# Kernel tuning notes

Hardware: AMD Instinct MI355X
Metric: run time of the kernel (lower is better)

The kernel has to match this reference:

```python
import jax, jax.numpy as jnp
import numpy as np
from jax import lax

B, N, H, D = 4, 384, 8, 5          # graphs, nodes/graph, heads, max multi-hop dist
NE, E_TOT, DH, L = 2048, 8192, 256, 10  # edges/graph, total real edges, d_hidden, curve samples
N_SPATIAL, N_EDGE_DIST = 64, 128


def _bn(x, g, b):
    # eval-mode BatchNorm1d (running_mean=0, running_var=1): affine only
    return x * g + b


def _conv1d(x, w):
    # x: [E, C, L], w: [O, I, 3], SAME padding, stride 1
    return lax.conv_general_dilated(x, w, (1,), 'SAME',
                                    dimension_numbers=('NCH', 'OIH', 'NCH'))


def setup_inputs() -> dict:
    key = jax.random.key(0)
    ks = iter(jax.random.split(key, 64))
    nrm = lambda shape, s=0.02: jax.random.normal(next(ks), shape, jnp.float32) * s
    std = 0.02 / np.sqrt(12.0)  # init_params with n_layer=12 for Linear weights
    inp = {}
    inp['attn_bias'] = jax.random.normal(next(ks), (B, N + 1, N + 1), jnp.float32)
    inp['spatial_pos'] = jax.random.randint(next(ks), (B, N, N), 0, N_SPATIAL)
    inp['d2_dist'] = jax.random.normal(next(ks), (B, N, N, 32), jnp.float32)
    inp['a3_dist'] = jax.random.normal(next(ks), (B, N, N, 32), jnp.float32)
    inp['edge_data'] = jax.random.normal(next(ks), (E_TOT, L, 7), jnp.float32)
    inp['edge_path'] = jax.random.randint(next(ks), (B, N, N, D), 0, NE + 1)
    inp['edge_padding_mask'] = jnp.zeros((B, NE), bool)  # all real edges
    inp['src'] = jax.random.randint(next(ks), (E_TOT,), 0, B * N)
    inp['dst'] = jax.random.randint(next(ks), (E_TOT,), 0, B * N)
    inp['node_data'] = jax.random.normal(next(ks), (B * N, DH), jnp.float32)
    # --- parameters ---
    inp['spatial_emb'] = nrm((N_SPATIAL, H)).at[0].set(0.0)  # padding_idx=0
    inp['t_virtual'] = nrm((1, H))
    inp['w_d2'] = nrm((H, 32), std); inp['b_d2'] = jnp.zeros((H,), jnp.float32)
    inp['w_a3'] = nrm((H, 32), std); inp['b_a3'] = jnp.zeros((H,), jnp.float32)
    inp['cw1'] = nrm((64, 7, 3), std);  inp['cg1'] = jnp.ones((64,));  inp['cb1'] = jnp.zeros((64,))
    inp['cw2'] = nrm((128, 64, 3), std); inp['cg2'] = jnp.ones((128,)); inp['cb2'] = jnp.zeros((128,))
    inp['cw3'] = nrm((256, 128, 3), std); inp['cg3'] = jnp.ones((256,)); inp['cb3'] = jnp.zeros((256,))
    inp['cw_out'] = nrm((H, 256), std)
    # _EdgeConv (UV-Net style): proj Linear(d_hidden->H), MLP(H->64->H), BN, GIN eps
    inp['wp'] = nrm((H, DH), std); inp['bp'] = jnp.zeros((H,))
    inp['w1'] = nrm((64, H), std); inp['b1'] = jnp.zeros((64,))
    inp['g1'] = jnp.ones((64,)); inp['bb1'] = jnp.zeros((64,))
    inp['w2'] = nrm((H, 64), std); inp['b2'] = jnp.zeros((H,))
    inp['g_out'] = jnp.ones((H,)); inp['bb_out'] = jnp.zeros((H,))
    inp['eps'] = jnp.zeros((), jnp.float32)
    inp['edge_dis_w'] = nrm((N_EDGE_DIST * H * H, 1))
    return inp


def reference(attn_bias, spatial_pos, d2_dist, a3_dist, edge_data, edge_path,
              edge_padding_mask, src, dst, node_data, spatial_emb, t_virtual,
              w_d2, b_d2, w_a3, b_a3, cw1, cg1, cb1, cw2, cg2, cb2, cw3, cg3, cb3,
              cw_out, wp, bp, w1, b1, g1, bb1, w2, b2, g_out, bb_out, eps, edge_dis_w):
    gab = jnp.repeat(attn_bias[:, None], H, axis=1)            # [B,H,N+1,N+1]
    spb = spatial_emb[spatial_pos]                              # [B,N,N,H]
    d2b = d2_dist @ w_d2.T + b_d2                               # [B,N,N,H]
    a3b = a3_dist @ w_a3.T + b_a3                               # [B,N,N,H]
    # CurveEncoder on per-edge curve samples
    x = jnp.transpose(edge_data, (0, 2, 1))                     # [E,7,L]
    x = jax.nn.leaky_relu(_bn(_conv1d(x, cw1), cg1[:, None], cb1[:, None]))
    x = jax.nn.leaky_relu(_bn(_conv1d(x, cw2), cg2[:, None], cb2[:, None]))
    x = jax.nn.leaky_relu(_bn(_conv1d(x, cw3), cg3[:, None], cb3[:, None]))
    ef = jnp.mean(x, axis=-1) @ cw_out.T                        # [E,H]
    # _EdgeConv: combine endpoint node features with edge features
    proj = node_data @ wp.T + bp                                # [B*N,H]
    h = (1.0 + eps) * ef + proj[src] + proj[dst]
    h = jax.nn.relu(_bn(h @ w1.T + b1, g1, bb1)) @ w2.T + b2
    edge_out = jax.nn.relu(_bn(h, g_out, bb_out))               # [E,H]
    # scatter real-edge features into padded table (row NE stays zero = padding)
    valid = (~edge_padding_mask).reshape(-1)                    # [B*NE]
    gidx = jnp.maximum(jnp.cumsum(valid) - 1, 0)
    vals = jnp.where(valid[:, None], edge_out[gidx], 0.0).reshape(B, NE, H)
    edge_feature = jnp.zeros((B, NE + 1, H), edge_out.dtype).at[:, :NE].set(vals)
    # gather along multi-hop paths, per-distance head mixing (bmm), normalize
    ep = edge_path.reshape(B, N * N * D)
    edge_input = jax.vmap(lambda f, p: f[p])(edge_feature, ep)  # [B,N*N*D,H]
    edge_input = edge_input.reshape(B, N, N, D, H)
    wdis = edge_dis_w.reshape(-1, H, H)[:D]                     # [D,H,H]
    edge_input = jnp.einsum('bijdh,dhk->bijdk', edge_input, wdis)
    sp = jnp.where(spatial_pos == 0, 1, spatial_pos)
    sp = jnp.where(sp > 1, sp - 1, sp)
    sp = jnp.clip(sp, 0, D)
    edge_bias = edge_input.sum(-2) / sp[..., None].astype(edge_input.dtype)
    inner = spb + d2b + a3b + edge_bias                         # [B,N,N,H]
    gab = gab.at[:, :, 1:, 1:].add(jnp.transpose(inner, (0, 3, 1, 2)))
    t = t_virtual.reshape(1, H, 1)
    gab = gab.at[:, :, 1:, 0].add(t)
    gab = gab.at[:, :, 0, :].add(t)
    return gab + attn_bias[:, None]
```

## Files before the change

### kernel.cpp

```cpp
#include <hip/hip_runtime.h>

#define NB    4
#define NNODE 384
#define NH    8
#define ND    5
#define NEDGE 2048
#define NEP1  2049
#define ETOT  8192
#define DHID  256
#define NP1   385
#define SQ1   (NP1*NP1)
#define NPOS  98304
#define NPOS2 (NPOS + 2)

typedef __attribute__((ext_vector_type(8)))  short short8;
typedef __attribute__((ext_vector_type(16))) float float16;

__device__ __forceinline__ unsigned short f2bf(float f) {
    union { float f; unsigned int u; } v; v.f = f;
    unsigned int u = v.u;
    return (unsigned short)((u + 0x7FFFu + ((u >> 16) & 1u)) >> 16);
}
__device__ __forceinline__ unsigned pkbf(float a, float b) {
    return (unsigned)f2bf(a) | ((unsigned)f2bf(b) << 16);
}
__device__ __forceinline__ short8 mk8(unsigned a, unsigned b, unsigned c, unsigned d) {
    union { unsigned u[4]; short8 s; } x; x.u[0]=a; x.u[1]=b; x.u[2]=c; x.u[3]=d; return x.s;
}
__device__ __forceinline__ float leaky(float v) { return v > 0.f ? v : 0.01f * v; }
__device__ __forceinline__ float16 zero16() {
    float16 z;
#pragma unroll
    for (int i = 0; i < 16; ++i) z[i] = 0.f;
    return z;
}
__device__ __forceinline__ void gl_lds16(const void* g, void* l) {
    __builtin_amdgcn_global_load_lds(
        (const __attribute__((address_space(1))) unsigned int*)g,
        (__attribute__((address_space(3))) unsigned int*)l,
        16, 0, 0);
}

__global__ __launch_bounds__(256) void prep_kernel(
    const float* __restrict__ cw1, const float* __restrict__ cw2, const float* __restrict__ cw3,
    const float* __restrict__ cw_out,
    const float* __restrict__ node_data, const float* __restrict__ wp, const float* __restrict__ bp,
    unsigned short* __restrict__ W1f, unsigned short* __restrict__ W2f, unsigned short* __restrict__ W3f,
    unsigned short* __restrict__ Wof,
    float* __restrict__ proj, float* __restrict__ edge_feature)
{
    int gid = blockIdx.x * 256 + threadIdx.x;
    if (gid < 98304) {
        int j = gid & 7, lane = (gid >> 3) & 63, blk = gid >> 9;
        int ks = blk & 7, tp = (blk >> 3) % 3, mt = blk / 24;
        int oc = mt * 32 + (lane & 31);
        int ic = ks * 16 + (lane >> 5) * 8 + j;
        W3f[gid] = f2bf(cw3[(oc * 128 + ic) * 3 + tp]);
    } else if (gid < 122880) {
        int f = gid - 98304;
        int j = f & 7, lane = (f >> 3) & 63, blk = f >> 9;
        int ks = blk & 3, tp = (blk >> 2) % 3, mt = blk / 12;
        int oc = mt * 32 + (lane & 31);
        int ic = ks * 16 + (lane >> 5) * 8 + j;
        W2f[f] = f2bf(cw2[(oc * 64 + ic) * 3 + tp]);
    } else if (gid < 124928) {
        int f = gid - 122880;
        int j = f & 7, lane = (f >> 3) & 63, blk = f >> 9;
        int ks = blk & 1, mt = blk >> 1;
        int oc = mt * 32 + (lane & 31);
        int k = ks * 16 + (lane >> 5) * 8 + j;
        int tp = k >> 3, c = k & 7;
        float v = (tp < 3 && c < 7) ? cw1[oc * 21 + c * 3 + tp] : 0.f;
        W1f[f] = f2bf(v);
    } else if (gid < 137216) {
        int f = gid - 124928;
        int v = f >> 3, h = f & 7;
        const float* nd = node_data + (size_t)v * DHID;
        const float* ww = wp + h * DHID;
        float acc = bp[h];
#pragma unroll 4
        for (int c = 0; c < DHID; c += 4)
            acc += nd[c]*ww[c] + nd[c+1]*ww[c+1] + nd[c+2]*ww[c+2] + nd[c+3]*ww[c+3];
        proj[f] = acc;
    } else if (gid < 137248) {
        int f = gid - 137216;
        int b = f >> 3, h = f & 7;
        edge_feature[((size_t)b * NEP1 + NEDGE) * NH + h] = 0.f;
    } else if (gid < 145440) {
        int f = gid - 137248;
        int j = f & 7, lane = (f >> 3) & 63, g = f >> 9;
        int m = lane & 31;
        int k = g * 16 + (lane >> 5) * 8 + j;
        Wof[f] = (m < 8) ? f2bf(cw_out[m * 256 + k]) : (unsigned short)0;
    }
}

#define X0_GROWS 8
__global__ __launch_bounds__(256) void pack_kernel(
    const float* __restrict__ edge_data,
    unsigned short* __restrict__ X0buf, unsigned short* __restrict__ X1buf,
    unsigned short* __restrict__ X2buf)
{
    int gid = blockIdx.x * 256 + threadIdx.x;
    const int NX0 = (NPOS + 2 * X0_GROWS) * 8;
    if (gid < NX0) {
        int row = gid >> 3, ch = gid & 7;
        int pos = row - X0_GROWS;
        unsigned short v = 0;
        if (pos >= 0 && pos < NPOS && ch < 7) {
            int pm = pos % 12;
            if (pm >= 1 && pm <= 10)
                v = f2bf(edge_data[(size_t)(pos / 12) * 70 + (pm - 1) * 7 + ch]);
        }
        X0buf[gid] = v;
    } else if (gid < NX0 + 128) {
        int f = gid - NX0;
        int p = f >> 5, rest = f & 31;
        int row = (rest >> 4) ? (NPOS + 1) : 0, col = rest & 15;
        X1buf[((size_t)p * NPOS2 + row) * 16 + col] = 0;
    } else if (gid < NX0 + 128 + 256) {
        int f = gid - NX0 - 128;
        int p = f >> 5, rest = f & 31;
        int row = (rest >> 4) ? (NPOS + 1) : 0, col = rest & 15;
        X2buf[((size_t)p * NPOS2 + row) * 16 + col] = 0;
    }
}

__global__ __launch_bounds__(256, 4) void conv1_kernel(
    const unsigned short* __restrict__ X0, const unsigned short* __restrict__ W1f,
    const float* __restrict__ cg1, const float* __restrict__ cb1,
    unsigned short* __restrict__ X1)
{
    const int t = threadIdx.x, wv = t >> 6, lane = t & 63;
    const int q = lane >> 5, n = lane & 31;
    const int pos = blockIdx.x * 128 + wv * 32 + n;

    float16 acc0 = zero16(), acc1 = zero16();
#pragma unroll
    for (int ks = 0; ks < 2; ++ks) {
        short8 b  = *(const short8*)(X0 + (pos - 1 + 2 * ks + q) * 8);
        short8 a0 = *(const short8*)(W1f + ((0 * 2 + ks) * 64 + lane) * 8);
        short8 a1 = *(const short8*)(W1f + ((1 * 2 + ks) * 64 + lane) * 8);
        acc0 = __builtin_amdgcn_mfma_f32_32x32x16_bf16(a0, b, acc0, 0, 0, 0);
        acc1 = __builtin_amdgcn_mfma_f32_32x32x16_bf16(a1, b, acc1, 0, 0, 0);
    }
    int pm = pos % 12;
    bool valid = (pm != 0) && (pm != 11);
#pragma unroll
    for (int mt = 0; mt < 2; ++mt) {
        const float16& acc = mt ? acc1 : acc0;
#pragma unroll
        for (int r2 = 0; r2 < 4; ++r2) {
            int oc0 = mt * 32 + 8 * r2 + 4 * q;
            float4 g4 = *(const float4*)(cg1 + oc0);
            float4 b4 = *(const float4*)(cb1 + oc0);
            unsigned short uu[4];
            uu[0] = valid ? f2bf(leaky(acc[r2*4+0] * g4.x + b4.x)) : (unsigned short)0;
            uu[1] = valid ? f2bf(leaky(acc[r2*4+1] * g4.y + b4.y)) : (unsigned short)0;
            uu[2] = valid ? f2bf(leaky(acc[r2*4+2] * g4.z + b4.z)) : (unsigned short)0;
            uu[3] = valid ? f2bf(leaky(acc[r2*4+3] * g4.w + b4.w)) : (unsigned short)0;
            uint2 pk; pk.x = uu[0] | ((unsigned)uu[1] << 16); pk.y = uu[2] | ((unsigned)uu[3] << 16);
            *(uint2*)(void*)(X1 + ((size_t)(oc0 >> 4) * NPOS2 + pos + 1) * 16 + (oc0 & 15)) = pk;
        }
    }
}

__global__ __launch_bounds__(256, 3) void conv2_kernel(
    const unsigned short* __restrict__ X1, const unsigned short* __restrict__ W2f,
    const float* __restrict__ cg2, const float* __restrict__ cb2,
    unsigned short* __restrict__ X2)
{
    __shared__ __align__(16) unsigned short sB[2][1568];
    const int t = threadIdx.x, wv = t >> 6, lane = t & 63;
    const int q = lane >> 5, n = lane & 31;
    const int base = blockIdx.x * 96;
    const int cbase = (wv < 3) ? wv * 64 : 132;

    gl_lds16(X1 + ((size_t)0 * NPOS2 + base) * 16 + (cbase + lane) * 8,
             &sB[0][cbase * 8]);

    float16 acc[3];
#pragma unroll
    for (int nt = 0; nt < 3; ++nt) acc[nt] = zero16();

    __syncthreads();

#pragma unroll
    for (int ks = 0; ks < 4; ++ks) {
        if (ks < 3)
            gl_lds16(X1 + ((size_t)(ks + 1) * NPOS2 + base) * 16 + (cbase + lane) * 8,
                     &sB[(ks + 1) & 1][cbase * 8]);
        const unsigned short* bb = sB[ks & 1];
#pragma unroll
        for (int tp = 0; tp < 3; ++tp) {
            short8 a = *(const short8*)(W2f + (((wv * 3 + tp) * 4 + ks) * 64 + lane) * 8);
#pragma unroll
            for (int nt = 0; nt < 3; ++nt) {
                short8 b = *(const short8*)(bb + (nt * 32 + n + tp) * 16 + q * 8);
                acc[nt] = __builtin_amdgcn_mfma_f32_32x32x16_bf16(a, b, acc[nt], 0, 0, 0);
            }
        }
        __syncthreads();
    }

#pragma unroll
    for (int nt = 0; nt < 3; ++nt) {
        int pos = base + nt * 32 + n;
        int pm = pos % 12;
        bool valid = (pm != 0) && (pm != 11);
#pragma unroll
        for (int r2 = 0; r2 < 4; ++r2) {
            int oc0 = wv * 32 + 8 * r2 + 4 * q;
            float4 g4 = *(const float4*)(cg2 + oc0);
            float4 b4 = *(const float4*)(cb2 + oc0);
            unsigned short uu[4];
            uu[0] = valid ? f2bf(leaky(acc[nt][r2*4+0] * g4.x + b4.x)) : (unsigned short)0;
            uu[1] = valid ? f2bf(leaky(acc[nt][r2*4+1] * g4.y + b4.y)) : (unsigned short)0;
            uu[2] = valid ? f2bf(leaky(acc[nt][r2*4+2] * g4.z + b4.z)) : (unsigned short)0;
            uu[3] = valid ? f2bf(leaky(acc[nt][r2*4+3] * g4.w + b4.w)) : (unsigned short)0;
            uint2 pk; pk.x = uu[0] | ((unsigned)uu[1] << 16); pk.y = uu[2] | ((unsigned)uu[3] << 16);
            *(uint2*)(void*)(X2 + ((size_t)(oc0 >> 4) * NPOS2 + pos + 1) * 16 + (oc0 & 15)) = pk;
        }
    }
}

__global__ __launch_bounds__(256, 2) void conv3_kernel(
    const unsigned short* __restrict__ X2, const unsigned short* __restrict__ W3f,
    const unsigned short* __restrict__ Wof,
    const float* __restrict__ cg3, const float* __restrict__ cb3,
    const int* __restrict__ src, const int* __restrict__ dst,
    const float* __restrict__ w1, const float* __restrict__ b1,
    const float* __restrict__ g1, const float* __restrict__ bb1,
    const float* __restrict__ w2, const float* __restrict__ b2,
    const float* __restrict__ g_out, const float* __restrict__ bb_out,
    const float* __restrict__ eps, const float* __restrict__ proj,
    float* __restrict__ edge_feature)
{
    __shared__ float fs[3072 + 64 + 512];
    __shared__ __align__(16) unsigned short sB[2][1568];
    const int t = threadIdx.x, wv = t >> 6, lane = t & 63;
    const int q = lane >> 5, n = lane & 31;
    const int base = blockIdx.x * 96;
    const int cbase = (wv < 3) ? wv * 64 : 132;

    gl_lds16(X2 + ((size_t)0 * NPOS2 + base) * 16 + (cbase + lane) * 8,
             &sB[0][cbase * 8]);

    float16 acc[2][3];
#pragma unroll
    for (int i = 0; i < 2; ++i)
#pragma unroll
        for (int nt = 0; nt < 3; ++nt) acc[i][nt] = zero16();

    __syncthreads();

#pragma unroll
    for (int ks = 0; ks < 8; ++ks) {
        if (ks < 7)
            gl_lds16(X2 + ((size_t)(ks + 1) * NPOS2 + base) * 16 + (cbase + lane) * 8,
                     &sB[(ks + 1) & 1][cbase * 8]);
        const unsigned short* bb = sB[ks & 1];
#pragma unroll
        for (int tp = 0; tp < 3; ++tp) {
            short8 a0 = *(const short8*)(W3f + ((((wv*2+0) * 3 + tp) * 8 + ks) * 64 + lane) * 8);
            short8 a1 = *(const short8*)(W3f + ((((wv*2+1) * 3 + tp) * 8 + ks) * 64 + lane) * 8);
#pragma unroll
            for (int nt = 0; nt < 3; ++nt) {
                short8 b = *(const short8*)(bb + (nt * 32 + n + tp) * 16 + q * 8);
                acc[0][nt] = __builtin_amdgcn_mfma_f32_32x32x16_bf16(a0, b, acc[0][nt], 0, 0, 0);
                acc[1][nt] = __builtin_amdgcn_mfma_f32_32x32x16_bf16(a1, b, acc[1][nt], 0, 0, 0);
            }
        }
        __syncthreads();
    }

    short8 wof[4];
#pragma unroll
    for (int g = 0; g < 4; ++g)
        wof[g] = *(const short8*)(Wof + ((wv * 4 + g) * 64 + lane) * 8);

#pragma unroll
    for (int nt = 0; nt < 3; ++nt) {
        int pm = (nt * 32 + n) % 12;
        bool valid = (pm != 0) && (pm != 11);
        float16 p = zero16();
#pragma unroll
        for (int i = 0; i < 2; ++i) {
            int mt = wv * 2 + i;
            float av[16];
#pragma unroll
            for (int r2 = 0; r2 < 4; ++r2) {
                int oc0 = mt * 32 + 8 * r2 + 4 * q;
                float4 g4 = *(const float4*)(cg3 + oc0);
                float4 b4 = *(const float4*)(cb3 + oc0);
                av[r2*4+0] = valid ? leaky(acc[i][nt][r2*4+0] * g4.x + b4.x) : 0.f;
                av[r2*4+1] = valid ? leaky(acc[i][nt][r2*4+1] * g4.y + b4.y) : 0.f;
                av[r2*4+2] = valid ? leaky(acc[i][nt][r2*4+2] * g4.z + b4.z) : 0.f;
                av[r2*4+3] = valid ? leaky(acc[i][nt][r2*4+3] * g4.w + b4.w) : 0.f;
            }
            unsigned pk[8], op[8];
#pragma unroll
            for (int z = 0; z < 8; ++z) pk[z] = pkbf(av[2*z], av[2*z+1]);
#pragma unroll
            for (int z = 0; z < 8; ++z) op[z] = __shfl_xor((int)pk[z], 32);
            short8 f0 = q == 0 ? mk8(pk[0], pk[1], op[0], op[1])
                               : mk8(op[2], op[3], pk[2], pk[3]);
            short8 f1 = q == 0 ? mk8(pk[4], pk[5], op[4], op[5])
                               : mk8(op[6], op[7], pk[6], pk[7]);
            p = __builtin_amdgcn_mfma_f32_32x32x16_bf16(wof[i*2+0], f0, p, 0, 0, 0);
            p = __builtin_amdgcn_mfma_f32_32x32x16_bf16(wof[i*2+1], f1, p, 0, 0, 0);
        }
        float4 st = make_float4(p[0], p[1], p[2], p[3]);
        *(float4*)&fs[((wv * 96) + nt * 32 + n) * 8 + 4 * q] = st;
    }
    __syncthreads();

    if (t < 64) {
        int e = t >> 3, h = t & 7;
        float s = 0.f;
#pragma unroll
        for (int w = 0; w < 4; ++w)
#pragma unroll 4
            for (int l = 0; l < 12; ++l) s += fs[(w * 96 + e * 12 + l) * 8 + h];
        float efv = 0.1f * s;
        int ge = blockIdx.x * 8 + e;
        fs[3072 + e * 8 + h] = (1.f + eps[0]) * efv
                             + proj[src[ge] * NH + h] + proj[dst[ge] * NH + h];
    }
    __syncthreads();

#pragma unroll
    for (int bb = 0; bb < 512; bb += 256) {
        int idx = bb + t;
        int e = idx >> 6, o = idx & 63;
        float a = b1[o];
#pragma unroll
        for (int h = 0; h < 8; ++h) a += fs[3072 + e * 8 + h] * w1[o * 8 + h];
        float v = a * g1[o] + bb1[o];
        fs[3136 + e * 64 + o] = v > 0.f ? v : 0.f;
    }
    __syncthreads();

    if (t < 64) {
        int e = t >> 3, h = t & 7;
        float a = b2[h];
#pragma unroll 8
        for (int o = 0; o < 64; ++o) a += fs[3136 + e * 64 + o] * w2[h * 64 + o];
        float v = a * g_out[h] + bb_out[h];
        v = v > 0.f ? v : 0.f;
        int ge = blockIdx.x * 8 + e;
        int b = ge >> 11, el2 = ge & (NEDGE - 1);
        edge_feature[((size_t)b * NEP1 + el2) * NH + h] = v;
    }
}

__global__ __launch_bounds__(256) void tbl_kernel(
    const float* __restrict__ edge_feature, const float* __restrict__ edge_dis_w,
    float* __restrict__ T)
{
    int idx = blockIdx.x * 256 + threadIdx.x;
    if (idx >= NEP1 * 8) return;
    int pi = idx >> 3, k = idx & 7;
    int d = blockIdx.y, b = blockIdx.z;
    const float* ef = edge_feature + ((size_t)b * NEP1 + pi) * NH;
    const float* w  = edge_dis_w + d * 64 + k;
    float s = 0.f;
#pragma unroll
    for (int h = 0; h < 8; ++h) s += ef[h] * w[h * 8];
    T[(((size_t)b * ND + d) * NEP1 + pi) * 8 + k] = s;
}

__global__ __launch_bounds__(256) void bias_kernel(
    const float* __restrict__ attn_bias, const int* __restrict__ spatial_pos,
    const float* __restrict__ d2_dist, const float* __restrict__ a3_dist,
    const int* __restrict__ edge_path,
    const float* __restrict__ spatial_emb, const float* __restrict__ t_virtual,
    const float* __restrict__ w_d2, const float* __restrict__ b_d2,
    const float* __restrict__ w_a3, const float* __restrict__ b_a3,
    const float* __restrict__ Tbl,
    float* __restrict__ out)
{
    __shared__ __align__(16) float s_emb[512];
    __shared__ __align__(16) float s_wd2[256];
    __shared__ __align__(16) float s_wa3[256];
    __shared__ float s_t[8], s_bd2[8], s_ba3[8];

    int t = threadIdx.x;
    for (int i = t; i < 512; i += 256) s_emb[i] = spatial_emb[i];
    if (t < 256) { s_wd2[t] = w_d2[t]; s_wa3[t] = w_a3[t]; }
    if (t < 8) { s_t[t] = t_virtual[t]; s_bd2[t] = b_d2[t]; s_ba3[t] = b_a3[t]; }
    __syncthreads();

    int gc = blockIdx.x * 32 + (t >> 3);
    int part = t & 7;
    if (gc >= NB * SQ1) return;
    int b   = gc / SQ1;
    int rem = gc % SQ1;
    int i = rem / NP1, j = rem % NP1;

    float base = 2.f * attn_bias[gc];
    bool border = (i == 0) || (j == 0);
    int r = border ? 0 : i - 1, c = border ? 0 : j - 1;
    size_t nidx = ((size_t)b * NNODE + r) * NNODE + c;
    int sp = spatial_pos[nidx];

    float acc[8];
    {
        float4 vd = ((const float4*)(d2_dist + nidx * 32))[part];
        float4 va = ((const float4*)(a3_dist + nidx * 32))[part];
        const float4* wd2 = (const float4*)s_wd2;
        const float4* wa3 = (const float4*)s_wa3;
#pragma unroll
        for (int h = 0; h < 8; ++h) {
            float4 w4 = wd2[h * 8 + part];
            float4 v4 = wa3[h * 8 + part];
            acc[h] = vd.x*w4.x + vd.y*w4.y + vd.z*w4.z + vd.w*w4.w
                   + va.x*v4.x + va.y*v4.y + va.z*v4.z + va.w*v4.w;
        }
    }

    float edp = 0.f;
    const int* ep = edge_path + nidx * ND;
    const float* Tb = Tbl + (size_t)b * (ND * NEP1 * 8);
#pragma unroll
    for (int d = 0; d < ND; ++d) {
        int pi = ep[d];
        edp += Tb[((size_t)d * NEP1 + pi) * 8 + part];
    }
    int spd = (sp == 0) ? 1 : sp;
    spd = (spd > 1) ? spd - 1 : spd;
    spd = (spd > ND) ? ND : spd;
    float inv = 1.f / (float)spd;

#pragma unroll
    for (int m = 1; m < 8; m <<= 1) {
#pragma unroll
        for (int h = 0; h < 8; ++h) acc[h] += __shfl_xor(acc[h], m, 64);
    }

    float val = border ? (base + s_t[part])
                       : (base + acc[part] + edp * inv
                          + s_emb[sp * 8 + part] + s_bd2[part] + s_ba3[part]);
    out[((size_t)b * NH + part) * SQ1 + (size_t)i * NP1 + j] = val;
}

extern "C" void kernel_launch(void* const* d_in, const int* in_sizes, int n_in,
                              void* d_out, int out_size, void* d_ws, size_t ws_size,
                              hipStream_t stream)
{
    const float* attn_bias   = (const float*)d_in[0];
    const int*   spatial_pos = (const int*)  d_in[1];
    const float* d2_dist     = (const float*)d_in[2];
    const float* a3_dist     = (const float*)d_in[3];
    const float* edge_data   = (const float*)d_in[4];
    const int*   edge_path   = (const int*)  d_in[5];
    const int*   src         = (const int*)  d_in[7];
    const int*   dst         = (const int*)  d_in[8];
    const float* node_data   = (const float*)d_in[9];
    const float* spatial_emb = (const float*)d_in[10];
    const float* t_virtual   = (const float*)d_in[11];
    const float* w_d2        = (const float*)d_in[12];
    const float* b_d2        = (const float*)d_in[13];
    const float* w_a3        = (const float*)d_in[14];
    const float* b_a3        = (const float*)d_in[15];
    const float* cw1         = (const float*)d_in[16];
    const float* cg1         = (const float*)d_in[17];
    const float* cb1         = (const float*)d_in[18];
    const float* cw2         = (const float*)d_in[19];
    const float* cg2         = (const float*)d_in[20];
    const float* cb2         = (const float*)d_in[21];
    const float* cw3         = (const float*)d_in[22];
    const float* cg3         = (const float*)d_in[23];
    const float* cb3         = (const float*)d_in[24];
    const float* cw_out      = (const float*)d_in[25];
    const float* wp          = (const float*)d_in[26];
    const float* bp          = (const float*)d_in[27];
    const float* w1          = (const float*)d_in[28];
    const float* b1          = (const float*)d_in[29];
    const float* g1          = (const float*)d_in[30];
    const float* bb1         = (const float*)d_in[31];
    const float* w2          = (const float*)d_in[32];
    const float* b2          = (const float*)d_in[33];
    const float* g_out       = (const float*)d_in[34];
    const float* bb_out      = (const float*)d_in[35];
    const float* eps         = (const float*)d_in[36];
    const float* edge_dis_w  = (const float*)d_in[37];

    float*          proj  = (float*)d_ws;
    float*          ef    = proj + NB * NNODE * NH;
    unsigned short* W1f   = (unsigned short*)(ef + NB * NEP1 * NH);
    unsigned short* W2f   = W1f + 2048;
    unsigned short* W3f   = W2f + 24576;
    unsigned short* Wof   = W3f + 98304;
    unsigned short* X0buf = Wof + 8192;
    unsigned short* X1buf = X0buf + (size_t)(NPOS + 2 * X0_GROWS) * 8;
    unsigned short* X2buf = X1buf + (size_t)4 * NPOS2 * 16;
    unsigned short* X0 = X0buf + X0_GROWS * 8;
    float*          Tbl   = (float*)X0buf;

    prep_kernel<<<569, 256, 0, stream>>>(cw1, cw2, cw3, cw_out, node_data, wp, bp,
                                         W1f, W2f, W3f, Wof, proj, ef);
    pack_kernel<<<3074, 256, 0, stream>>>(edge_data, X0buf, X1buf, X2buf);

    conv1_kernel<<<NPOS / 128, 256, 0, stream>>>(X0, W1f, cg1, cb1, X1buf);
    conv2_kernel<<<NPOS / 96, 256, 0, stream>>>(X1buf, W2f, cg2, cb2, X2buf);
    conv3_kernel<<<NPOS / 96, 256, 0, stream>>>(X2buf, W3f, Wof, cg3, cb3,
                                                src, dst, w1, b1, g1, bb1,
                                                w2, b2, g_out, bb_out, eps,
                                                proj, ef);

    dim3 tgrid((NEP1 * 8 + 255) / 256, ND, NB);
    tbl_kernel<<<tgrid, 256, 0, stream>>>(ef, edge_dis_w, Tbl);

    int nbias = (NB * SQ1 * 8 + 255) / 256;
    bias_kernel<<<nbias, 256, 0, stream>>>(
        attn_bias, spatial_pos, d2_dist, a3_dist, edge_path,
        spatial_emb, t_virtual, w_d2, b_d2, w_a3, b_a3,
        Tbl, (float*)d_out);
}
```

Before: 355.6 us.

## Split d2/a3 projection into separate kernel, load all conv K-slices upfront

Moves the d2/a3 distance projection out of bias_kernel into a new eins_kernel. It reduces with a butterfly shuffle and stores one bf16 value per head and cell, reusing the X1 buffer once conv2 has consumed it. conv2 and conv3 now prefetch every K-slice into shared memory in one go instead of double-buffering with a barrier per step, and their occupancy bounds are raised. conv3 aliases its epilogue float buffer onto the same shared memory, the node projection is vectorized with float4, and the bf16 rounding of the d2/a3 term is a small precision loss.

After: 370.1 us. +4.1%, slower.

```diff
diff --git a/kernel.cpp b/kernel.cpp
--- a/kernel.cpp
+++ b/kernel.cpp
@@ -12,6 +12,7 @@
 #define SQ1   (NP1*NP1)
 #define NPOS  98304
 #define NPOS2 (NPOS + 2)
+#define NCELL (NB*NNODE*NNODE)
 
 typedef __attribute__((ext_vector_type(8)))  short short8;
 typedef __attribute__((ext_vector_type(16))) float float16;
@@ -20,6 +21,9 @@
     union { float f; unsigned int u; } v; v.f = f;
     unsigned int u = v.u;
     return (unsigned short)((u + 0x7FFFu + ((u >> 16) & 1u)) >> 16);
+}
+__device__ __forceinline__ float bf2f(unsigned short s) {
+    union { unsigned int u; float f; } v; v.u = ((unsigned int)s) << 16; return v.f;
 }
 __device__ __forceinline__ unsigned pkbf(float a, float b) {
     return (unsigned)f2bf(a) | ((unsigned)f2bf(b) << 16);
@@ -75,13 +79,21 @@
     } else if (gid < 137216) {
         int f = gid - 124928;
         int v = f >> 3, h = f & 7;
-        const float* nd = node_data + (size_t)v * DHID;
-        const float* ww = wp + h * DHID;
-        float acc = bp[h];
+        const float4* nd4 = (const float4*)(node_data + (size_t)v * DHID);
+        const float4* ww4 = (const float4*)(wp + (size_t)h * DHID);
+        float s0 = 0.f, s1 = 0.f, s2 = 0.f, s3 = 0.f;
 #pragma unroll 4
-        for (int c = 0; c < DHID; c += 4)
-            acc += nd[c]*ww[c] + nd[c+1]*ww[c+1] + nd[c+2]*ww[c+2] + nd[c+3]*ww[c+3];
-        proj[f] = acc;
+        for (int c = 0; c < 64; c += 4) {
+            float4 x0 = nd4[c+0], y0 = ww4[c+0];
+            float4 x1 = nd4[c+1], y1 = ww4[c+1];
+            float4 x2 = nd4[c+2], y2 = ww4[c+2];
+            float4 x3 = nd4[c+3], y3 = ww4[c+3];
+            s0 += x0.x*y0.x + x0.y*y0.y + x0.z*y0.z + x0.w*y0.w;
+            s1 += x1.x*y1.x + x1.y*y1.y + x1.z*y1.z + x1.w*y1.w;
+            s2 += x2.x*y2.x + x2.y*y2.y + x2.z*y2.z + x2.w*y2.w;
+            s3 += x3.x*y3.x + x3.y*y3.y + x3.z*y3.z + x3.w*y3.w;
+        }
+        proj[f] = bp[h] + (s0 + s1) + (s2 + s3);
     } else if (gid < 137248) {
         int f = gid - 137216;
         int b = f >> 3, h = f & 7;
@@ -165,19 +177,21 @@
     }
 }
 
-__global__ __launch_bounds__(256, 3) void conv2_kernel(
+__global__ __launch_bounds__(256, 4) void conv2_kernel(
     const unsigned short* __restrict__ X1, const unsigned short* __restrict__ W2f,
     const float* __restrict__ cg2, const float* __restrict__ cb2,
     unsigned short* __restrict__ X2)
 {
-    __shared__ __align__(16) unsigned short sB[2][1568];
+    __shared__ __align__(16) unsigned short sB[4][1568];
     const int t = threadIdx.x, wv = t >> 6, lane = t & 63;
     const int q = lane >> 5, n = lane & 31;
     const int base = blockIdx.x * 96;
     const int cbase = (wv < 3) ? wv * 64 : 132;
 
-    gl_lds16(X1 + ((size_t)0 * NPOS2 + base) * 16 + (cbase + lane) * 8,
-             &sB[0][cbase * 8]);
+#pragma unroll
+    for (int ks = 0; ks < 4; ++ks)
+        gl_lds16(X1 + ((size_t)ks * NPOS2 + base) * 16 + (cbase + lane) * 8,
+                 &sB[ks][cbase * 8]);
 
     float16 acc[3];
 #pragma unroll
@@ -186,22 +200,16 @@
     __syncthreads();
 
 #pragma unroll
-    for (int ks = 0; ks < 4; ++ks) {
-        if (ks < 3)
-            gl_lds16(X1 + ((size_t)(ks + 1) * NPOS2 + base) * 16 + (cbase + lane) * 8,
-                     &sB[(ks + 1) & 1][cbase * 8]);
-        const unsigned short* bb = sB[ks & 1];
+    for (int ks = 0; ks < 4; ++ks)
 #pragma unroll
         for (int tp = 0; tp < 3; ++tp) {
             short8 a = *(const short8*)(W2f + (((wv * 3 + tp) * 4 + ks) * 64 + lane) * 8);
 #pragma unroll
             for (int nt = 0; nt < 3; ++nt) {
-                short8 b = *(const short8*)(bb + (nt * 32 + n + tp) * 16 + q * 8);
+                short8 b = *(const short8*)(&sB[ks][(nt * 32 + n + tp) * 16 + q * 8]);
                 acc[nt] = __builtin_amdgcn_mfma_f32_32x32x16_bf16(a, b, acc[nt], 0, 0, 0);
             }
         }
-        __syncthreads();
-    }
 
 #pragma unroll
     for (int nt = 0; nt < 3; ++nt) {
@@ -224,7 +232,7 @@
     }
 }
 
-__global__ __launch_bounds__(256, 2) void conv3_kernel(
+__global__ __launch_bounds__(256, 3) void conv3_kernel(
     const unsigned short* __restrict__ X2, const unsigned short* __restrict__ W3f,
     const unsigned short* __restrict__ Wof,
     const float* __restrict__ cg3, const float* __restrict__ cb3,
@@ -236,15 +244,18 @@
     const float* __restrict__ eps, const float* __restrict__ proj,
     float* __restrict__ edge_feature)
 {
-    __shared__ float fs[3072 + 64 + 512];
-    __shared__ __align__(16) unsigned short sB[2][1568];
+    __shared__ __align__(16) unsigned char smem3[25088];
+    unsigned short* sB = (unsigned short*)smem3;
+    float* fs = (float*)smem3;
     const int t = threadIdx.x, wv = t >> 6, lane = t & 63;
     const int q = lane >> 5, n = lane & 31;
     const int base = blockIdx.x * 96;
     const int cbase = (wv < 3) ? wv * 64 : 132;
 
-    gl_lds16(X2 + ((size_t)0 * NPOS2 + base) * 16 + (cbase + lane) * 8,
-             &sB[0][cbase * 8]);
+#pragma unroll
+    for (int ks = 0; ks < 8; ++ks)
+        gl_lds16(X2 + ((size_t)ks * NPOS2 + base) * 16 + (cbase + lane) * 8,
+                 &sB[ks * 1568 + cbase * 8]);
 
     float16 acc[2][3];
 #pragma unroll
@@ -255,24 +266,20 @@
     __syncthreads();
 
 #pragma unroll
-    for (int ks = 0; ks < 8; ++ks) {
-        if (ks < 7)
-            gl_lds16(X2 + ((size_t)(ks + 1) * NPOS2 + base) * 16 + (cbase + lane) * 8,
-                     &sB[(ks + 1) & 1][cbase * 8]);
-        const unsigned short* bb = sB[ks & 1];
+    for (int ks = 0; ks < 8; ++ks)
 #pragma unroll
         for (int tp = 0; tp < 3; ++tp) {
             short8 a0 = *(const short8*)(W3f + ((((wv*2+0) * 3 + tp) * 8 + ks) * 64 + lane) * 8);
             short8 a1 = *(const short8*)(W3f + ((((wv*2+1) * 3 + tp) * 8 + ks) * 64 + lane) * 8);
 #pragma unroll
             for (int nt = 0; nt < 3; ++nt) {
-                short8 b = *(const short8*)(bb + (nt * 32 + n + tp) * 16 + q * 8);
+                short8 b = *(const short8*)(&sB[ks * 1568 + (nt * 32 + n + tp) * 16 + q * 8]);
                 acc[0][nt] = __builtin_amdgcn_mfma_f32_32x32x16_bf16(a0, b, acc[0][nt], 0, 0, 0);
                 acc[1][nt] = __builtin_amdgcn_mfma_f32_32x32x16_bf16(a1, b, acc[1][nt], 0, 0, 0);
             }
         }
-        __syncthreads();
-    }
+
+    __syncthreads();
 
     short8 wof[4];
 #pragma unroll
@@ -354,6 +361,43 @@
     }
 }
 
+__global__ __launch_bounds__(256) void eins_kernel(
+    const float* __restrict__ d2_dist, const float* __restrict__ a3_dist,
+    const float* __restrict__ w_d2, const float* __restrict__ w_a3,
+    unsigned short* __restrict__ acc8)
+{
+    __shared__ __align__(16) float s_wd2[256];
+    __shared__ __align__(16) float s_wa3[256];
+    int t = threadIdx.x;
+    s_wd2[t] = w_d2[t]; s_wa3[t] = w_a3[t];
+    __syncthreads();
+
+    const int part = t & 7;
+    const bool pb0 = part & 1, pb1 = (part >> 1) & 1, pb2 = (part >> 2) & 1;
+    size_t cell = (size_t)blockIdx.x * 32 + (t >> 3);
+
+    float4 vd = ((const float4*)(d2_dist + cell * 32))[part];
+    float4 va = ((const float4*)(a3_dist + cell * 32))[part];
+
+    float acc[8];
+#pragma unroll
+    for (int h = 0; h < 8; ++h) {
+        float4 w4 = ((const float4*)s_wd2)[h * 8 + part];
+        float4 v4 = ((const float4*)s_wa3)[h * 8 + part];
+        acc[h] = vd.x*w4.x + vd.y*w4.y + vd.z*w4.z + vd.w*w4.w
+               + va.x*v4.x + va.y*v4.y + va.z*v4.z + va.w*v4.w;
+    }
+    float y0 = (pb0 ? acc[1] : acc[0]) + __shfl_xor(pb0 ? acc[0] : acc[1], 1, 64);
+    float y1 = (pb0 ? acc[3] : acc[2]) + __shfl_xor(pb0 ? acc[2] : acc[3], 1, 64);
+    float y2 = (pb0 ? acc[5] : acc[4]) + __shfl_xor(pb0 ? acc[4] : acc[5], 1, 64);
+    float y3 = (pb0 ? acc[7] : acc[6]) + __shfl_xor(pb0 ? acc[6] : acc[7], 1, 64);
+    float z0 = (pb1 ? y1 : y0) + __shfl_xor(pb1 ? y0 : y1, 2, 64);
+    float z1 = (pb1 ? y3 : y2) + __shfl_xor(pb1 ? y2 : y3, 2, 64);
+    float rr = (pb2 ? z1 : z0) + __shfl_xor(pb2 ? z0 : z1, 4, 64);
+
+    acc8[cell * 8 + part] = f2bf(rr);
+}
+
 __global__ __launch_bounds__(256) void tbl_kernel(
     const float* __restrict__ edge_feature, const float* __restrict__ edge_dis_w,
     float* __restrict__ T)
@@ -372,22 +416,17 @@
 
 __global__ __launch_bounds__(256) void bias_kernel(
     const float* __restrict__ attn_bias, const int* __restrict__ spatial_pos,
-    const float* __restrict__ d2_dist, const float* __restrict__ a3_dist,
     const int* __restrict__ edge_path,
     const float* __restrict__ spatial_emb, const float* __restrict__ t_virtual,
-    const float* __restrict__ w_d2, const float* __restrict__ b_d2,
-    const float* __restrict__ w_a3, const float* __restrict__ b_a3,
-    const float* __restrict__ Tbl,
+    const float* __restrict__ b_d2, const float* __restrict__ b_a3,
+    const float* __restrict__ Tbl, const unsigned short* __restrict__ acc8,
     float* __restrict__ out)
 {
-    __shared__ __align__(16) float s_emb[512];
-    __shared__ __align__(16) float s_wd2[256];
-    __shared__ __align__(16) float s_wa3[256];
+    __shared__ float s_emb[512];
     __shared__ float s_t[8], s_bd2[8], s_ba3[8];
 
     int t = threadIdx.x;
     for (int i = t; i < 512; i += 256) s_emb[i] = spatial_emb[i];
-    if (t < 256) { s_wd2[t] = w_d2[t]; s_wa3[t] = w_a3[t]; }
     if (t < 8) { s_t[t] = t_virtual[t]; s_bd2[t] = b_d2[t]; s_ba3[t] = b_a3[t]; }
     __syncthreads();
 
@@ -404,20 +443,7 @@
     size_t nidx = ((size_t)b * NNODE + r) * NNODE + c;
     int sp = spatial_pos[nidx];
 
-    float acc[8];
-    {
-        float4 vd = ((const float4*)(d2_dist + nidx * 32))[part];
-        float4 va = ((const float4*)(a3_dist + nidx * 32))[part];
-        const float4* wd2 = (const float4*)s_wd2;
-        const float4* wa3 = (const float4*)s_wa3;
-#pragma unroll
-        for (int h = 0; h < 8; ++h) {
-            float4 w4 = wd2[h * 8 + part];
-            float4 v4 = wa3[h * 8 + part];
-            acc[h] = vd.x*w4.x + vd.y*w4.y + vd.z*w4.z + vd.w*w4.w
-                   + va.x*v4.x + va.y*v4.y + va.z*v4.z + va.w*v4.w;
-        }
-    }
+    float accv = bf2f(acc8[nidx * 8 + part]);
 
     float edp = 0.f;
     const int* ep = edge_path + nidx * ND;
@@ -432,14 +458,8 @@
     spd = (spd > ND) ? ND : spd;
     float inv = 1.f / (float)spd;
 
-#pragma unroll
-    for (int m = 1; m < 8; m <<= 1) {
-#pragma unroll
-        for (int h = 0; h < 8; ++h) acc[h] += __shfl_xor(acc[h], m, 64);
-    }
-
     float val = border ? (base + s_t[part])
-                       : (base + acc[part] + edp * inv
+                       : (base + accv + edp * inv
                           + s_emb[sp * 8 + part] + s_bd2[part] + s_ba3[part]);
     out[((size_t)b * NH + part) * SQ1 + (size_t)i * NP1 + j] = val;
 }
@@ -497,6 +517,7 @@
     unsigned short* X2buf = X1buf + (size_t)4 * NPOS2 * 16;
     unsigned short* X0 = X0buf + X0_GROWS * 8;
     float*          Tbl   = (float*)X0buf;
+    unsigned short* acc8  = X1buf;
 
     prep_kernel<<<569, 256, 0, stream>>>(cw1, cw2, cw3, cw_out, node_data, wp, bp,
                                          W1f, W2f, W3f, Wof, proj, ef);
@@ -504,6 +525,9 @@
 
     conv1_kernel<<<NPOS / 128, 256, 0, stream>>>(X0, W1f, cg1, cb1, X1buf);
     conv2_kernel<<<NPOS / 96, 256, 0, stream>>>(X1buf, W2f, cg2, cb2, X2buf);
+
+    eins_kernel<<<NCELL / 32, 256, 0, stream>>>(d2_dist, a3_dist, w_d2, w_a3, acc8);
+
     conv3_kernel<<<NPOS / 96, 256, 0, stream>>>(X2buf, W3f, Wof, cg3, cb3,
                                                 src, dst, w1, b1, g1, bb1,
                                                 w2, b2, g_out, bb_out, eps,
@@ -514,7 +538,7 @@
 
     int nbias = (NB * SQ1 * 8 + 255) / 256;
     bias_kernel<<<nbias, 256, 0, stream>>>(
-        attn_bias, spatial_pos, d2_dist, a3_dist, edge_path,
-        spatial_emb, t_virtual, w_d2, b_d2, w_a3, b_a3,
-        Tbl, (float*)d_out);
-}
+        attn_bias, spatial_pos, edge_path,
+        spatial_emb, t_virtual, b_d2, b_a3,
+        Tbl, acc8, (float*)d_out);
+}
```
